# Optimization experiments

Hardware: AMD Instinct MI355X
Metric: run time of the kernel (lower is better)

Reference implementation:

```python
import jax, jax.numpy as jnp
import numpy as np

N, E = 50000, 400000
IC, OC, WIDTH, DEPTH = 128, 128, 2, 3


def setup_inputs() -> dict:
    key = jax.random.key(0)
    ks = jax.random.split(key, 9)
    s = 0.02
    return {
        "node_tensor": jax.random.normal(ks[0], (N, 1, IC), jnp.float32),
        "edge_index": jax.random.randint(ks[1], (2, E), 0, N, dtype=jnp.int32),
        "W_pre": jax.random.normal(ks[2], (IC, OC * WIDTH), jnp.float32) * s,
        "b_pre": jax.random.normal(ks[3], (OC * WIDTH,), jnp.float32) * s,
        "W_merge": jax.random.normal(ks[4], (IC, OC * WIDTH), jnp.float32) * s,
        "b_merge": jax.random.normal(ks[5], (OC * WIDTH,), jnp.float32) * s,
        "W_conv": jax.random.normal(ks[6], (WIDTH, OC, OC), jnp.float32) * s,
        "b_conv": jax.random.normal(ks[7], (OC * WIDTH,), jnp.float32) * s,
    }


def reference(node_tensor, edge_index, W_pre, b_pre, W_merge, b_merge, W_conv, b_conv):
    n = node_tensor.shape[0]
    nodes = node_tensor[:, 0, :]                       # (N, IC)

    src, dst = edge_index[0], edge_index[1]
    deg = jax.ops.segment_sum(jnp.ones((E,), node_tensor.dtype), dst, num_segments=n)
    norm = jnp.where(deg > 0, jax.lax.rsqrt(jnp.maximum(deg, 1.0)), 0.0)  # D^{-1/2}

    def laplacian_action(x):                           # x: (N, C); L_sym x
        agg = jax.ops.segment_sum(norm[src, None] * x[src], dst, num_segments=n)
        return x - norm[:, None] * agg

    merge = nodes @ W_merge + b_merge                  # (N, OC*W)
    out = jax.nn.relu(nodes @ W_pre + b_pre + merge)   # (N, OC*W)

    for _ in range(DEPTH - 1):
        out = out - laplacian_action(out)
        # grouped 1x1 conv: width contiguous groups of OC channels
        h = out.reshape(n, WIDTH, OC)
        h = jnp.einsum("nwi,woi->nwo", h, W_conv).reshape(n, WIDTH * OC) + b_conv
        out = jax.nn.relu(h + merge)

    # final (N, OC, W) reshape + adaptive_avg_pool1d(1) == mean over width
    out = out.reshape(n, OC, WIDTH).mean(axis=-1)
    return out[:, :, None]                             # (N, OC, 1)
```

## Files before the change

kernel.cpp:

```cpp
#include <hip/hip_runtime.h>

typedef unsigned short u16;
typedef __attribute__((ext_vector_type(8))) short bf16x8;
typedef __attribute__((ext_vector_type(4))) float f32x4;

#define ICNST 128
#define C2 256

__device__ __forceinline__ float bf2f(u16 u){
  return __uint_as_float(((unsigned int)u) << 16);
}
__device__ __forceinline__ float2 bf2x2(unsigned int u){
  float2 r;
  r.x = __uint_as_float(u << 16);
  r.y = __uint_as_float(u & 0xffff0000u);
  return r;
}
__device__ __forceinline__ u16 f2bf(float f){
  unsigned int u = __float_as_uint(f);
  unsigned int r = (u + 0x7fffu + ((u >> 16) & 1u)) >> 16;
  return (u16)r;
}
__device__ __forceinline__ unsigned int pk2(float a, float b){
  return (unsigned int)f2bf(a) | ((unsigned int)f2bf(b) << 16);
}

__global__ __launch_bounds__(256) void k_pre(const int* __restrict__ dst,
    int* __restrict__ deg, const float* __restrict__ Wpre,
    const float* __restrict__ Wmrg, const float* __restrict__ Wcv,
    u16* __restrict__ WT, u16* __restrict__ Wc, int E){
  int bid = blockIdx.x;
  if (bid < 384){
    int idx = bid * 256 + threadIdx.x;
    if (idx < 65536){
      int j = idx & 511, k = idx >> 9;
      float v = (j < 256) ? Wpre[k * 256 + j] : Wmrg[k * 256 + (j - 256)];
      WT[j * 128 + k] = f2bf(v);
    } else if (idx < 65536 + 32768){
      int x = idx - 65536;
      Wc[x] = f2bf(Wcv[x]);
    }
  } else {
    int e = (bid - 384) * 256 + threadIdx.x;
    if (e < E) atomicAdd(&deg[dst[e]], 1);
  }
}

__global__ __launch_bounds__(256) void k_scan1(const int* __restrict__ deg,
    int* __restrict__ bsum, int n){
  __shared__ int red[256];
  int t = threadIdx.x;
  int i = blockIdx.x * 256 + t;
  red[t] = (i < n) ? deg[i] : 0;
  __syncthreads();
  for (int off = 128; off > 0; off >>= 1){
    if (t < off) red[t] += red[t + off];
    __syncthreads();
  }
  if (t == 0) bsum[blockIdx.x] = red[0];
}

__global__ __launch_bounds__(256) void k_scan2(int* __restrict__ bsum, int nb){
  __shared__ int s[256];
  int t = threadIdx.x;
  int v = (t < nb) ? bsum[t] : 0;
  s[t] = v;
  __syncthreads();
  for (int off = 1; off < 256; off <<= 1){
    int u = (t >= off) ? s[t - off] : 0;
    __syncthreads();
    s[t] += u;
    __syncthreads();
  }
  if (t < nb) bsum[t] = s[t] - v;
}

__global__ __launch_bounds__(256) void k_scan3(const int* __restrict__ deg,
    const int* __restrict__ bsum, int* __restrict__ row_start,
    int* __restrict__ cursor, float* __restrict__ norm, int n){
  __shared__ int s[256];
  int t = threadIdx.x;
  int i = blockIdx.x * 256 + t;
  int v = (i < n) ? deg[i] : 0;
  s[t] = v;
  __syncthreads();
  for (int off = 1; off < 256; off <<= 1){
    int u = (t >= off) ? s[t - off] : 0;
    __syncthreads();
    s[t] += u;
    __syncthreads();
  }
  int ex = s[t] - v + bsum[blockIdx.x];
  if (i < n){
    row_start[i] = ex;
    cursor[i] = ex;
    norm[i] = (v > 0) ? rsqrtf((float)v) : 0.f;
    if (i == n - 1) row_start[n] = ex + v;
  }
}

__global__ void k_scatter(const int* __restrict__ src, const int* __restrict__ dstA,
    int* __restrict__ cursor, int* __restrict__ csr_src, int E){
  int e = blockIdx.x * blockDim.x + threadIdx.x;
  if (e < E){
    int d = dstA[e];
    int pos = atomicAdd(&cursor[d], 1);
    csr_src[pos] = src[e];
  }
}

__global__ __launch_bounds__(512) void k_initM(const float* __restrict__ node,
    const u16* __restrict__ WT, const float* __restrict__ bpre,
    const float* __restrict__ bmrg, const float* __restrict__ norm,
    u16* __restrict__ merge, u16* __restrict__ outA, int n){
  __shared__ u16 Al[64 * 128];
  int t = threadIdx.x;
  int w = t >> 6, l = t & 63;
  int n0 = blockIdx.x * 64;
  int cb = w * 32;
  int lk = (l >> 4) * 8;

  bf16x8 breg[4][4];
  #pragma unroll
  for (int ks = 0; ks < 4; ++ks)
    #pragma unroll
    for (int fc = 0; fc < 4; ++fc){
      int j = (fc < 2) ? (cb + fc * 16 + (l & 15))
                       : (256 + cb + (fc - 2) * 16 + (l & 15));
      breg[ks][fc] = *(const bf16x8*)(WT + (size_t)j * 128 + ks * 32 + lk);
    }
  float nr4[4];
  #pragma unroll
  for (int fr = 0; fr < 4; ++fr){
    int row = n0 + fr * 16 + (l & 15);
    nr4[fr] = (row < n) ? norm[row] : 0.f;
  }
  float4 bPr[2], bMr[2];
  #pragma unroll
  for (int fcp = 0; fcp < 2; ++fcp){
    int j0 = cb + fcp * 16 + (l >> 4) * 4;
    bPr[fcp] = *(const float4*)(bpre + j0);
    bMr[fcp] = *(const float4*)(bmrg + j0);
  }

  {
    int row = t >> 3, c0 = (t & 7) * 16;
    const float* src = node + (size_t)(n0 + row) * ICNST + c0;
    bool ok = (n0 + row) < n;
    #pragma unroll
    for (int q = 0; q < 4; ++q){
      float4 v = ok ? *(const float4*)(src + q * 4) : float4{0.f, 0.f, 0.f, 0.f};
      int byte = (row * 256 + c0 * 2 + q * 8) ^ ((row & 7) << 4);
      uint2 pp; pp.x = pk2(v.x, v.y); pp.y = pk2(v.z, v.w);
      *(uint2*)((char*)Al + byte) = pp;
    }
  }
  __syncthreads();

  f32x4 acc[4][4] = {};
  #pragma unroll
  for (int ks = 0; ks < 4; ++ks){
    bf16x8 af[4];
    #pragma unroll
    for (int fr = 0; fr < 4; ++fr){
      int row = fr * 16 + (l & 15);
      int byte = (row * 256 + ks * 64 + (l >> 4) * 16) ^ ((l & 7) << 4);
      af[fr] = *(const bf16x8*)((const char*)Al + byte);
    }
    #pragma unroll
    for (int fr = 0; fr < 4; ++fr)
      #pragma unroll
      for (int fc = 0; fc < 4; ++fc)
        acc[fr][fc] = __builtin_amdgcn_mfma_f32_16x16x32_bf16(breg[ks][fc], af[fr], acc[fr][fc], 0, 0, 0);
  }

  #pragma unroll
  for (int fr = 0; fr < 4; ++fr){
    int row = n0 + fr * 16 + (l & 15);
    bool ok = row < n;
    float nr = nr4[fr];
    #pragma unroll
    for (int fcp = 0; fcp < 2; ++fcp){
      int j0 = cb + fcp * 16 + (l >> 4) * 4;
      f32x4 aP = acc[fr][fcp], aM = acc[fr][fcp + 2];
      float bPe[4] = {bPr[fcp].x, bPr[fcp].y, bPr[fcp].z, bPr[fcp].w};
      float bMe[4] = {bMr[fcp].x, bMr[fcp].y, bMr[fcp].z, bMr[fcp].w};
      ushort4 mgv, outv;
      u16* mgp = (u16*)&mgv; u16* otp = (u16*)&outv;
      #pragma unroll
      for (int r = 0; r < 4; ++r){
        float mg = aM[r] + bMe[r];
        float o  = aP[r] + bPe[r] + mg;
        o = (o > 0.f) ? o : 0.f;
        mgp[r] = f2bf(mg);
        otp[r] = f2bf(nr * o);
      }
      if (ok){
        *(ushort4*)(merge + (size_t)row * C2 + j0) = mgv;
        *(ushort4*)(outA  + (size_t)row * C2 + j0) = outv;
      }
    }
  }
}

template<int FINAL>
__global__ __launch_bounds__(512) void k_convM(u16* __restrict__ buf,
    const u16* __restrict__ Wc, const float* __restrict__ bc,
    const u16* __restrict__ merge, const float* __restrict__ norm,
    float* __restrict__ out, int n){
  __shared__ u16 Al[64 * 256];
  int t = threadIdx.x;
  int w = t >> 6, l = t & 63;
  int n0 = blockIdx.x * 64;
  int wh = w >> 2;
  int lk = (l >> 4) * 8;

  bf16x8 breg[4][2];
  #pragma unroll
  for (int ks = 0; ks < 4; ++ks)
    #pragma unroll
    for (int fc = 0; fc < 2; ++fc){
      int rw = w * 32 + fc * 16 + (l & 15);
      breg[ks][fc] = *(const bf16x8*)(Wc + (size_t)rw * 128 + ks * 32 + lk);
    }
  float nr4[4];
  #pragma unroll
  for (int fr = 0; fr < 4; ++fr){
    int row = n0 + fr * 16 + (l & 15);
    nr4[fr] = (row < n) ? norm[row] : 0.f;
  }
  float4 bCr[2];
  ushort4 mgr[4][2];
  #pragma unroll
  for (int fc = 0; fc < 2; ++fc)
    bCr[fc] = *(const float4*)(bc + w * 32 + fc * 16 + (l >> 4) * 4);
  #pragma unroll
  for (int fr = 0; fr < 4; ++fr){
    int row = n0 + fr * 16 + (l & 15);
    bool ok = row < n;
    #pragma unroll
    for (int fc = 0; fc < 2; ++fc){
      int j0 = w * 32 + fc * 16 + (l >> 4) * 4;
      mgr[fr][fc] = ok ? *(const ushort4*)(merge + (size_t)row * C2 + j0)
                       : ushort4{0, 0, 0, 0};
    }
  }

  {
    int row = t >> 3, c0 = (t & 7) * 32;
    const u16* src = buf + (size_t)(n0 + row) * C2 + c0;
    bool ok = (n0 + row) < n;
    #pragma unroll
    for (int q = 0; q < 4; ++q){
      uint4 v = ok ? *(const uint4*)(src + q * 8) : uint4{0u, 0u, 0u, 0u};
      int byte = (row * 512 + c0 * 2 + q * 16) ^ ((row & 7) << 4);
      *(uint4*)((char*)Al + byte) = v;
    }
  }
  __syncthreads();

  f32x4 acc[4][2] = {};
  #pragma unroll
  for (int ks = 0; ks < 4; ++ks){
    bf16x8 af[4];
    #pragma unroll
    for (int fr = 0; fr < 4; ++fr){
      int row = fr * 16 + (l & 15);
      int byte = (row * 512 + wh * 256 + ks * 64 + (l >> 4) * 16) ^ ((l & 7) << 4);
      af[fr] = *(const bf16x8*)((const char*)Al + byte);
    }
    #pragma unroll
    for (int fr = 0; fr < 4; ++fr)
      #pragma unroll
      for (int fc = 0; fc < 2; ++fc)
        acc[fr][fc] = __builtin_amdgcn_mfma_f32_16x16x32_bf16(breg[ks][fc], af[fr], acc[fr][fc], 0, 0, 0);
  }

  #pragma unroll
  for (int fr = 0; fr < 4; ++fr){
    int row = n0 + fr * 16 + (l & 15);
    bool ok = row < n;
    float nr = nr4[fr];
    #pragma unroll
    for (int fc = 0; fc < 2; ++fc){
      int j0 = w * 32 + fc * 16 + (l >> 4) * 4;
      float bCe[4] = {bCr[fc].x, bCr[fc].y, bCr[fc].z, bCr[fc].w};
      const u16* mge = (const u16*)&mgr[fr][fc];
      float v[4];
      #pragma unroll
      for (int r = 0; r < 4; ++r){
        float o = acc[fr][fc][r] + bCe[r] + bf2f(mge[r]);
        v[r] = (o > 0.f) ? o : 0.f;
      }
      if (!FINAL){
        ushort4 ov;
        u16* ovp = (u16*)&ov;
        #pragma unroll
        for (int r = 0; r < 4; ++r) ovp[r] = f2bf(nr * v[r]);
        if (ok) *(ushort4*)(buf + (size_t)row * C2 + j0) = ov;
      } else {
        float2 om;
        om.x = 0.5f * (v[0] + v[1]);
        om.y = 0.5f * (v[2] + v[3]);
        if (ok) *(float2*)(out + (size_t)row * 128 + (j0 >> 1)) = om;
      }
    }
  }
}

__global__ __launch_bounds__(256) void k_prop(const u16* __restrict__ A, u16* __restrict__ B,
    const int* __restrict__ row_start, const int* __restrict__ csr,
    const float* __restrict__ norm, int n){
  int wid = (blockIdx.x * 256 + threadIdx.x) >> 6;
  int lane = threadIdx.x & 63;
  int half = lane >> 5, c = lane & 31;
  int gw = wid * 2 + half;
  if (gw >= n) return;
  int b = row_start[gw], e = row_start[gw + 1];
  float a0 = 0.f, a1 = 0.f, a2 = 0.f, a3 = 0.f, a4 = 0.f, a5 = 0.f, a6 = 0.f, a7 = 0.f;
  const u16* Ac = A + (size_t)c * 8;
  int j = b;
  for (; j + 4 <= e; j += 4){
    int s0 = csr[j], s1 = csr[j + 1], s2 = csr[j + 2], s3 = csr[j + 3];
    uint4 r0 = *(const uint4*)(Ac + (size_t)s0 * C2);
    uint4 r1 = *(const uint4*)(Ac + (size_t)s1 * C2);
    uint4 r2 = *(const uint4*)(Ac + (size_t)s2 * C2);
    uint4 r3 = *(const uint4*)(Ac + (size_t)s3 * C2);
    float2 p;
    p = bf2x2(r0.x); a0 += p.x; a1 += p.y; p = bf2x2(r0.y); a2 += p.x; a3 += p.y;
    p = bf2x2(r0.z); a4 += p.x; a5 += p.y; p = bf2x2(r0.w); a6 += p.x; a7 += p.y;
    p = bf2x2(r1.x); a0 += p.x; a1 += p.y; p = bf2x2(r1.y); a2 += p.x; a3 += p.y;
    p = bf2x2(r1.z); a4 += p.x; a5 += p.y; p = bf2x2(r1.w); a6 += p.x; a7 += p.y;
    p = bf2x2(r2.x); a0 += p.x; a1 += p.y; p = bf2x2(r2.y); a2 += p.x; a3 += p.y;
    p = bf2x2(r2.z); a4 += p.x; a5 += p.y; p = bf2x2(r2.w); a6 += p.x; a7 += p.y;
    p = bf2x2(r3.x); a0 += p.x; a1 += p.y; p = bf2x2(r3.y); a2 += p.x; a3 += p.y;
    p = bf2x2(r3.z); a4 += p.x; a5 += p.y; p = bf2x2(r3.w); a6 += p.x; a7 += p.y;
  }
  for (; j < e; ++j){
    int s0 = csr[j];
    uint4 r0 = *(const uint4*)(Ac + (size_t)s0 * C2);
    float2 p;
    p = bf2x2(r0.x); a0 += p.x; a1 += p.y; p = bf2x2(r0.y); a2 += p.x; a3 += p.y;
    p = bf2x2(r0.z); a4 += p.x; a5 += p.y; p = bf2x2(r0.w); a6 += p.x; a7 += p.y;
  }
  float nd = norm[gw];
  uint4 ov;
  ov.x = pk2(nd * a0, nd * a1);
  ov.y = pk2(nd * a2, nd * a3);
  ov.z = pk2(nd * a4, nd * a5);
  ov.w = pk2(nd * a6, nd * a7);
  *(uint4*)(B + (size_t)gw * C2 + c * 8) = ov;
}

extern "C" void kernel_launch(void* const* d_in, const int* in_sizes, int n_in,
                              void* d_out, int out_size, void* d_ws, size_t ws_size,
                              hipStream_t stream){
  const float* node = (const float*)d_in[0];
  const int*   eidx = (const int*)d_in[1];
  const float* Wpre = (const float*)d_in[2];
  const float* bpre = (const float*)d_in[3];
  const float* Wmrg = (const float*)d_in[4];
  const float* bmrg = (const float*)d_in[5];
  const float* Wcv  = (const float*)d_in[6];
  const float* bcv  = (const float*)d_in[7];
  float* out = (float*)d_out;

  const int n = in_sizes[0] / ICNST;
  const int E = in_sizes[1] / 2;
  const int* srcp = eidx;
  const int* dstp = eidx + E;

  char* ws = (char*)d_ws;
  size_t off = 0;
  auto alloc = [&](size_t bytes) -> char* {
    char* p = ws + off;
    off += bytes;
    off = (off + 255) & ~(size_t)255;
    return p;
  };
  int*   deg       = (int*)  alloc((size_t)n * 4);
  float* norm      = (float*)alloc((size_t)n * 4);
  int*   row_start = (int*)  alloc((size_t)(n + 1) * 4);
  int*   cursor    = (int*)  alloc((size_t)n * 4);
  int*   csr       = (int*)  alloc((size_t)E * 4);
  u16*   merge     = (u16*)  alloc((size_t)n * C2 * 2);
  u16*   bufA      = (u16*)  alloc((size_t)n * C2 * 2);
  u16*   bufB      = (u16*)  alloc((size_t)n * C2 * 2);
  u16*   WT        = (u16*)  alloc((size_t)512 * 128 * 2);
  u16*   Wcbf      = (u16*)  alloc((size_t)2 * 128 * 128 * 2);
  int*   bsum      = (int*)  alloc((size_t)256 * 4);
  (void)ws_size; (void)n_in; (void)out_size;

  const int nb = (n + 255) / 256;

  hipMemsetAsync(deg, 0, (size_t)n * 4, stream);
  k_pre<<<384 + (E + 255) / 256, 256, 0, stream>>>(dstp, deg, Wpre, Wmrg, Wcv, WT, Wcbf, E);
  k_scan1<<<nb, 256, 0, stream>>>(deg, bsum, n);
  k_scan2<<<1, 256, 0, stream>>>(bsum, nb);
  k_scan3<<<nb, 256, 0, stream>>>(deg, bsum, row_start, cursor, norm, n);
  k_scatter<<<(E + 255) / 256, 256, 0, stream>>>(srcp, dstp, cursor, csr, E);

  int gb64 = (n + 63) / 64;
  k_initM<<<gb64, 512, 0, stream>>>(node, WT, bpre, bmrg, norm, merge, bufA, n);

  k_prop<<<(n + 7) / 8, 256, 0, stream>>>(bufA, bufB, row_start, csr, norm, n);
  k_convM<0><<<gb64, 512, 0, stream>>>(bufB, Wcbf, bcv, merge, norm, nullptr, n);
  k_prop<<<(n + 7) / 8, 256, 0, stream>>>(bufB, bufA, row_start, csr, norm, n);
  k_convM<1><<<gb64, 512, 0, stream>>>(bufA, Wcbf, bcv, merge, norm, out, n);
}
```

Measured before the change: 214.9 us.

## Stage GEMM epilogues through LDS for coalesced row stores and merge loads

The init and conv kernels now write their epilogue results (merge, the scaled activations, the next buffer or the final pooled output) into a swizzled LDS tile. After a barrier, that tile is written to global memory as full 16-byte row-contiguous chunks instead of scattered 8-byte per-fragment stores. The conv kernel also loads the merge tile coalesced into LDS alongside the activation tile, rather than doing per-fragment global reads. Weight fragments are loaded inside the k-loop instead of being preloaded for all k-steps, which lowers register pressure. The cost is extra LDS (up to 64 KB per block), which may cut occupancy, plus additional barriers and LDS round trips.

```diff
diff --git a/kernel.cpp b/kernel.cpp
--- a/kernel.cpp
+++ b/kernel.cpp
@@ -114,21 +114,13 @@
     const float* __restrict__ bmrg, const float* __restrict__ norm,
     u16* __restrict__ merge, u16* __restrict__ outA, int n){
   __shared__ u16 Al[64 * 128];
+  __shared__ u16 Ep[64 * 256];
   int t = threadIdx.x;
   int w = t >> 6, l = t & 63;
   int n0 = blockIdx.x * 64;
   int cb = w * 32;
   int lk = (l >> 4) * 8;
 
-  bf16x8 breg[4][4];
-  #pragma unroll
-  for (int ks = 0; ks < 4; ++ks)
-    #pragma unroll
-    for (int fc = 0; fc < 4; ++fc){
-      int j = (fc < 2) ? (cb + fc * 16 + (l & 15))
-                       : (256 + cb + (fc - 2) * 16 + (l & 15));
-      breg[ks][fc] = *(const bf16x8*)(WT + (size_t)j * 128 + ks * 32 + lk);
-    }
   float nr4[4];
   #pragma unroll
   for (int fr = 0; fr < 4; ++fr){
@@ -160,6 +152,13 @@
   f32x4 acc[4][4] = {};
   #pragma unroll
   for (int ks = 0; ks < 4; ++ks){
+    bf16x8 bf[4];
+    #pragma unroll
+    for (int fc = 0; fc < 4; ++fc){
+      int j = (fc < 2) ? (cb + fc * 16 + (l & 15))
+                       : (256 + cb + (fc - 2) * 16 + (l & 15));
+      bf[fc] = *(const bf16x8*)(WT + (size_t)j * 128 + ks * 32 + lk);
+    }
     bf16x8 af[4];
     #pragma unroll
     for (int fr = 0; fr < 4; ++fr){
@@ -171,13 +170,13 @@
     for (int fr = 0; fr < 4; ++fr)
       #pragma unroll
       for (int fc = 0; fc < 4; ++fc)
-        acc[fr][fc] = __builtin_amdgcn_mfma_f32_16x16x32_bf16(breg[ks][fc], af[fr], acc[fr][fc], 0, 0, 0);
-  }
-
+        acc[fr][fc] = __builtin_amdgcn_mfma_f32_16x16x32_bf16(bf[fc], af[fr], acc[fr][fc], 0, 0, 0);
+  }
+
+  ushort4 outv[4][2];
   #pragma unroll
   for (int fr = 0; fr < 4; ++fr){
-    int row = n0 + fr * 16 + (l & 15);
-    bool ok = row < n;
+    int rl = fr * 16 + (l & 15);
     float nr = nr4[fr];
     #pragma unroll
     for (int fcp = 0; fcp < 2; ++fcp){
@@ -185,8 +184,8 @@
       f32x4 aP = acc[fr][fcp], aM = acc[fr][fcp + 2];
       float bPe[4] = {bPr[fcp].x, bPr[fcp].y, bPr[fcp].z, bPr[fcp].w};
       float bMe[4] = {bMr[fcp].x, bMr[fcp].y, bMr[fcp].z, bMr[fcp].w};
-      ushort4 mgv, outv;
-      u16* mgp = (u16*)&mgv; u16* otp = (u16*)&outv;
+      ushort4 mgv;
+      u16* mgp = (u16*)&mgv; u16* otp = (u16*)&outv[fr][fcp];
       #pragma unroll
       for (int r = 0; r < 4; ++r){
         float mg = aM[r] + bMe[r];
@@ -195,11 +194,40 @@
         mgp[r] = f2bf(mg);
         otp[r] = f2bf(nr * o);
       }
-      if (ok){
-        *(ushort4*)(merge + (size_t)row * C2 + j0) = mgv;
-        *(ushort4*)(outA  + (size_t)row * C2 + j0) = outv;
-      }
-    }
+      int byte = (rl * 512 + j0 * 2) ^ ((rl & 7) << 4);
+      *(ushort4*)((char*)Ep + byte) = mgv;
+    }
+  }
+  __syncthreads();
+  #pragma unroll
+  for (int round = 0; round < 4; ++round){
+    int idx = round * 512 + t;
+    int rl = idx >> 5, off = (idx & 31) * 16;
+    int byte = (rl * 512 + off) ^ ((rl & 7) << 4);
+    uint4 v = *(const uint4*)((const char*)Ep + byte);
+    if (n0 + rl < n)
+      *(uint4*)((char*)merge + (size_t)(n0 + rl) * 512 + off) = v;
+  }
+  __syncthreads();
+  #pragma unroll
+  for (int fr = 0; fr < 4; ++fr){
+    int rl = fr * 16 + (l & 15);
+    #pragma unroll
+    for (int fcp = 0; fcp < 2; ++fcp){
+      int j0 = cb + fcp * 16 + (l >> 4) * 4;
+      int byte = (rl * 512 + j0 * 2) ^ ((rl & 7) << 4);
+      *(ushort4*)((char*)Ep + byte) = outv[fr][fcp];
+    }
+  }
+  __syncthreads();
+  #pragma unroll
+  for (int round = 0; round < 4; ++round){
+    int idx = round * 512 + t;
+    int rl = idx >> 5, off = (idx & 31) * 16;
+    int byte = (rl * 512 + off) ^ ((rl & 7) << 4);
+    uint4 v = *(const uint4*)((const char*)Ep + byte);
+    if (n0 + rl < n)
+      *(uint4*)((char*)outA + (size_t)(n0 + rl) * 512 + off) = v;
   }
 }
 
@@ -209,20 +237,13 @@
     const u16* __restrict__ merge, const float* __restrict__ norm,
     float* __restrict__ out, int n){
   __shared__ u16 Al[64 * 256];
+  __shared__ u16 Ep[64 * 256];
   int t = threadIdx.x;
   int w = t >> 6, l = t & 63;
   int n0 = blockIdx.x * 64;
   int wh = w >> 2;
   int lk = (l >> 4) * 8;
 
-  bf16x8 breg[4][2];
-  #pragma unroll
-  for (int ks = 0; ks < 4; ++ks)
-    #pragma unroll
-    for (int fc = 0; fc < 2; ++fc){
-      int rw = w * 32 + fc * 16 + (l & 15);
-      breg[ks][fc] = *(const bf16x8*)(Wc + (size_t)rw * 128 + ks * 32 + lk);
-    }
   float nr4[4];
   #pragma unroll
   for (int fr = 0; fr < 4; ++fr){
@@ -230,31 +251,22 @@
     nr4[fr] = (row < n) ? norm[row] : 0.f;
   }
   float4 bCr[2];
-  ushort4 mgr[4][2];
   #pragma unroll
   for (int fc = 0; fc < 2; ++fc)
     bCr[fc] = *(const float4*)(bc + w * 32 + fc * 16 + (l >> 4) * 4);
-  #pragma unroll
-  for (int fr = 0; fr < 4; ++fr){
-    int row = n0 + fr * 16 + (l & 15);
-    bool ok = row < n;
-    #pragma unroll
-    for (int fc = 0; fc < 2; ++fc){
-      int j0 = w * 32 + fc * 16 + (l >> 4) * 4;
-      mgr[fr][fc] = ok ? *(const ushort4*)(merge + (size_t)row * C2 + j0)
-                       : ushort4{0, 0, 0, 0};
-    }
-  }
 
   {
     int row = t >> 3, c0 = (t & 7) * 32;
-    const u16* src = buf + (size_t)(n0 + row) * C2 + c0;
     bool ok = (n0 + row) < n;
+    const u16* srcA = buf   + (size_t)(n0 + row) * C2 + c0;
+    const u16* srcM = merge + (size_t)(n0 + row) * C2 + c0;
     #pragma unroll
     for (int q = 0; q < 4; ++q){
-      uint4 v = ok ? *(const uint4*)(src + q * 8) : uint4{0u, 0u, 0u, 0u};
+      uint4 va = ok ? *(const uint4*)(srcA + q * 8) : uint4{0u, 0u, 0u, 0u};
       int byte = (row * 512 + c0 * 2 + q * 16) ^ ((row & 7) << 4);
-      *(uint4*)((char*)Al + byte) = v;
+      *(uint4*)((char*)Al + byte) = va;
+      uint4 vm = ok ? *(const uint4*)(srcM + q * 8) : uint4{0u, 0u, 0u, 0u};
+      *(uint4*)((char*)Ep + byte) = vm;
     }
   }
   __syncthreads();
@@ -262,6 +274,12 @@
   f32x4 acc[4][2] = {};
   #pragma unroll
   for (int ks = 0; ks < 4; ++ks){
+    bf16x8 bf[2];
+    #pragma unroll
+    for (int fc = 0; fc < 2; ++fc){
+      int rw = w * 32 + fc * 16 + (l & 15);
+      bf[fc] = *(const bf16x8*)(Wc + (size_t)rw * 128 + ks * 32 + lk);
+    }
     bf16x8 af[4];
     #pragma unroll
     for (int fr = 0; fr < 4; ++fr){
@@ -273,19 +291,20 @@
     for (int fr = 0; fr < 4; ++fr)
       #pragma unroll
       for (int fc = 0; fc < 2; ++fc)
-        acc[fr][fc] = __builtin_amdgcn_mfma_f32_16x16x32_bf16(breg[ks][fc], af[fr], acc[fr][fc], 0, 0, 0);
+        acc[fr][fc] = __builtin_amdgcn_mfma_f32_16x16x32_bf16(bf[fc], af[fr], acc[fr][fc], 0, 0, 0);
   }
 
   #pragma unroll
   for (int fr = 0; fr < 4; ++fr){
-    int row = n0 + fr * 16 + (l & 15);
-    bool ok = row < n;
+    int rl = fr * 16 + (l & 15);
     float nr = nr4[fr];
     #pragma unroll
     for (int fc = 0; fc < 2; ++fc){
       int j0 = w * 32 + fc * 16 + (l >> 4) * 4;
+      int byte = (rl * 512 + j0 * 2) ^ ((rl & 7) << 4);
+      ushort4 mg4 = *(const ushort4*)((const char*)Ep + byte);
+      const u16* mge = (const u16*)&mg4;
       float bCe[4] = {bCr[fc].x, bCr[fc].y, bCr[fc].z, bCr[fc].w};
-      const u16* mge = (const u16*)&mgr[fr][fc];
       float v[4];
       #pragma unroll
       for (int r = 0; r < 4; ++r){
@@ -297,14 +316,25 @@
         u16* ovp = (u16*)&ov;
         #pragma unroll
         for (int r = 0; r < 4; ++r) ovp[r] = f2bf(nr * v[r]);
-        if (ok) *(ushort4*)(buf + (size_t)row * C2 + j0) = ov;
+        *(ushort4*)((char*)Ep + byte) = ov;
       } else {
         float2 om;
         om.x = 0.5f * (v[0] + v[1]);
         om.y = 0.5f * (v[2] + v[3]);
-        if (ok) *(float2*)(out + (size_t)row * 128 + (j0 >> 1)) = om;
+        *(float2*)((char*)Ep + byte) = om;
       }
     }
+  }
+  __syncthreads();
+  char* dstBase = FINAL ? (char*)out : (char*)buf;
+  #pragma unroll
+  for (int round = 0; round < 4; ++round){
+    int idx = round * 512 + t;
+    int rl = idx >> 5, off = (idx & 31) * 16;
+    int byte = (rl * 512 + off) ^ ((rl & 7) << 4);
+    uint4 v = *(const uint4*)((const char*)Ep + byte);
+    if (n0 + rl < n)
+      *(uint4*)(dstBase + (size_t)(n0 + rl) * 512 + off) = v;
   }
 }
 
```

Result: faster. 210.3 us (-2.1%).
